# Kernel tuning notes

Hardware: AMD Instinct MI355X
Metric: run time of the kernel (lower is better)

The kernel has to match this reference:

```python
import jax, jax.numpy as jnp
import numpy as np
from jax import lax

C = 256
K = 7
PAD = (K - 1) // 2
EMB = 128
MULT = 4
HID = C * MULT
B = 16
L = 4096
EPS = 1e-6
LAYER_SCALE_INIT = 1e-6


def setup_inputs() -> dict:
    key = jax.random.key(0)
    ks = jax.random.split(key, 10)
    x = jax.random.normal(ks[0], (B, C, L), dtype=jnp.float32)
    t = jax.random.normal(ks[1], (B, EMB), dtype=jnp.float32)
    # depthwise conv: Conv1d(C, C, K, groups=C) -> weight [C, 1, K]
    dw_w = jax.random.normal(ks[2], (C, 1, K), dtype=jnp.float32) * 0.1
    dw_b = jax.random.normal(ks[3], (C,), dtype=jnp.float32) * 0.02
    # FiLM linear: Linear(EMB, 2C)
    film_w = jax.random.normal(ks[4], (2 * C, EMB), dtype=jnp.float32) * 0.05
    film_b = jax.random.normal(ks[5], (2 * C,), dtype=jnp.float32) * 0.02
    # pointwise 1x1 convs
    pw1_w = jax.random.normal(ks[6], (HID, C), dtype=jnp.float32) * 0.05
    pw1_b = jax.random.normal(ks[7], (HID,), dtype=jnp.float32) * 0.02
    pw2_w = jax.random.normal(ks[8], (C, HID), dtype=jnp.float32) * 0.05
    pw2_b = jax.random.normal(ks[9], (C,), dtype=jnp.float32) * 0.02
    gamma = jnp.full((C, 1), LAYER_SCALE_INIT, dtype=jnp.float32)
    return {"x": x, "t": t, "dw_w": dw_w, "dw_b": dw_b,
            "film_w": film_w, "film_b": film_b,
            "pw1_w": pw1_w, "pw1_b": pw1_b,
            "pw2_w": pw2_w, "pw2_b": pw2_b, "gamma": gamma}


def reference(x, t, dw_w, dw_b, film_w, film_b, pw1_w, pw1_b, pw2_w, pw2_b, gamma):
    # circular pad on spatial dim, then valid depthwise conv
    xp = jnp.concatenate([x[..., -PAD:], x, x[..., :PAD]], axis=-1)  # [B, C, L+2*PAD]
    y = lax.conv_general_dilated(
        xp, dw_w, window_strides=(1,), padding='VALID',
        dimension_numbers=('NCH', 'OIH', 'NCH'),
        feature_group_count=C) + dw_b[:, None]                       # [B, C, L]
    # GroupNorm(1, C, affine=False): normalize over (C, L) per sample
    mu = jnp.mean(y, axis=(1, 2), keepdims=True)
    var = jnp.mean(jnp.square(y - mu), axis=(1, 2), keepdims=True)
    yn = (y - mu) * lax.rsqrt(var + EPS)
    # FiLM: scale/shift from embedded time
    ss = t @ film_w.T + film_b                                       # [B, 2C]
    scale, shift = jnp.split(ss, 2, axis=1)                          # [B, C] each
    yn = yn * (scale[:, :, None] + 1.0) + shift[:, :, None]
    # pointwise mixing with ReLU
    h = jax.nn.relu(jnp.einsum('bcl,dc->bdl', yn, pw1_w) + pw1_b[:, None])  # [B, HID, L]
    branch = jnp.einsum('bdl,cd->bcl', h, pw2_w) + pw2_b[:, None]           # [B, C, L]
    # layerscale + residual
    return x + branch * gamma
```

## Files before the change

### kernel.cpp

```cpp
#include <hip/hip_runtime.h>

typedef short s16x8 __attribute__((ext_vector_type(8)));
typedef short s16x4 __attribute__((ext_vector_type(4)));
typedef float f32x4 __attribute__((ext_vector_type(4)));

#define NB 16
#define NC 256
#define NL 4096
#define NH 1024
#define NE 128

#define WS_YNT   0ull
#define WS_PW1   33554432ull
#define WS_PW2   34078720ull
#define WS_AF    34603008ull
#define WS_BF    34619392ull
#define WS_SUMS  34635776ull

#define MFMA16(a, b, c) __builtin_amdgcn_mfma_f32_16x16x32_bf16((a), (b), (c), 0, 0, 0)

static __device__ __forceinline__ short f2bf(float f) {
    unsigned int u = __float_as_uint(f);
    u = (u + 0x7fffu + ((u >> 16) & 1u)) >> 16;
    return (short)u;
}
static __device__ __forceinline__ float bf2f(short s) {
    return __uint_as_float(((unsigned int)(unsigned short)s) << 16);
}

__global__ __launch_bounds__(256) void k0_prep(const float* __restrict__ pw1,
                                               const float* __restrict__ pw2,
                                               short* __restrict__ pw1b,
                                               short* __restrict__ pw2b,
                                               float* __restrict__ sums) {
    int idx = blockIdx.x * 256 + threadIdx.x;
    if (idx < NH * NC) {
        pw1b[idx] = f2bf(pw1[idx]);
        pw2b[idx] = f2bf(pw2[idx]);
    }
    if (blockIdx.x == 0 && threadIdx.x < 32) sums[threadIdx.x] = 0.f;
}

__global__ __launch_bounds__(256) void k1_dwconv(const float* __restrict__ x,
                                                 const float* __restrict__ dw_w,
                                                 const float* __restrict__ dw_b,
                                                 short* __restrict__ ynt,
                                                 float* __restrict__ sums) {
    __shared__ float xt[64][81];
    __shared__ float red1[4], red2[4];
    const int b = blockIdx.x >> 8;
    const int rem = blockIdx.x & 255;
    const int c0 = (rem >> 6) << 6;
    const int l0 = (rem & 63) << 6;
    const int t = threadIdx.x;

    const float* xb = x + ((size_t)(b * NC + c0)) * NL;
    {
#pragma unroll
        for (int j = 0; j < 5; ++j) {
            const int idx = t + 256 * j;
            const int row = idx / 20;
            const int col = idx - row * 20;
            const int lg = (l0 - 4 + col * 4) & (NL - 1);
            const float4 v = *(const float4*)(xb + (size_t)row * NL + lg);
            xt[row][col * 4 + 0] = v.x;
            xt[row][col * 4 + 1] = v.y;
            xt[row][col * 4 + 2] = v.z;
            xt[row][col * 4 + 3] = v.w;
        }
    }

    const int c = t & 63;
    const int w = t >> 6;
    const float w0 = dw_w[(c0 + c) * 7 + 0], w1 = dw_w[(c0 + c) * 7 + 1],
                w2 = dw_w[(c0 + c) * 7 + 2], w3 = dw_w[(c0 + c) * 7 + 3],
                w4 = dw_w[(c0 + c) * 7 + 4], w5 = dw_w[(c0 + c) * 7 + 5],
                w6 = dw_w[(c0 + c) * 7 + 6];
    const float bb = dw_b[c0 + c];
    __syncthreads();

    float win0 = xt[c][w * 16 + 1], win1 = xt[c][w * 16 + 2], win2 = xt[c][w * 16 + 3],
          win3 = xt[c][w * 16 + 4], win4 = xt[c][w * 16 + 5], win5 = xt[c][w * 16 + 6],
          win6 = xt[c][w * 16 + 7];
    float s1 = 0.f, s2 = 0.f;
    short* yo = ynt + ((size_t)(b * NL + l0 + w * 16)) * NC + c0 + c;
#pragma unroll
    for (int i = 0; i < 16; ++i) {
        const float y = bb + w0 * win0 + w1 * win1 + w2 * win2 + w3 * win3 +
                        w4 * win4 + w5 * win5 + w6 * win6;
        s1 += y;
        s2 += y * y;
        yo[(size_t)i * NC] = f2bf(y);
        win0 = win1; win1 = win2; win2 = win3; win3 = win4; win4 = win5; win5 = win6;
        win6 = xt[c][w * 16 + i + 8];
    }
    for (int off = 32; off; off >>= 1) {
        s1 += __shfl_down(s1, off, 64);
        s2 += __shfl_down(s2, off, 64);
    }
    if ((t & 63) == 0) { red1[w] = s1; red2[w] = s2; }
    __syncthreads();
    if (t == 0) {
        atomicAdd(&sums[b * 2 + 0], red1[0] + red1[1] + red1[2] + red1[3]);
        atomicAdd(&sums[b * 2 + 1], red2[0] + red2[1] + red2[2] + red2[3]);
    }
}

__global__ __launch_bounds__(256) void k2_finalize(const float* __restrict__ tin,
                                                   const float* __restrict__ fw,
                                                   const float* __restrict__ fb,
                                                   const float* __restrict__ sums,
                                                   float* __restrict__ afilm,
                                                   float* __restrict__ bfilm) {
    const int b = blockIdx.x;
    const int c = threadIdx.x;
    const float n = (float)(NC * NL);
    const float mu = sums[2 * b] / n;
    const float var = sums[2 * b + 1] / n - mu * mu;
    const float rs = rsqrtf(var + 1e-6f);

    const f32x4* tv = (const f32x4*)(tin + b * NE);
    const f32x4* wA = (const f32x4*)(fw + (size_t)c * NE);
    const f32x4* wB = (const f32x4*)(fw + (size_t)(NC + c) * NE);
    float sc = 0.f, sh = 0.f;
#pragma unroll
    for (int e = 0; e < NE / 4; ++e) {
        f32x4 tq = tv[e], aq = wA[e], bq = wB[e];
        sc += tq[0] * aq[0] + tq[1] * aq[1] + tq[2] * aq[2] + tq[3] * aq[3];
        sh += tq[0] * bq[0] + tq[1] * bq[1] + tq[2] * bq[2] + tq[3] * bq[3];
    }
    sc += fb[c];
    sh += fb[NC + c];
    const float A = rs * (1.f + sc);
    afilm[b * NC + c] = A;
    bfilm[b * NC + c] = sh - mu * A;
}

__global__ __launch_bounds__(256, 2) void k3_gemm(
    const short* __restrict__ ynt, const short* __restrict__ pw1b,
    const short* __restrict__ pw2b, const float* __restrict__ pb1,
    const float* __restrict__ pb2, const float* __restrict__ afilm,
    const float* __restrict__ bfilm, const float* __restrict__ gamma,
    const float* __restrict__ x, float* __restrict__ out) {
    __shared__ short yn[64 * 264];
    __shared__ short hs[2][64 * 136];

    const int b = blockIdx.x >> 6;
    const int l0 = (blockIdx.x & 63) << 6;
    const int t = threadIdx.x;
    const int lane = t & 63, wid = t >> 6;
    const int ln = lane & 15, quad = lane >> 4;

    {
        const int c8 = (t & 31) * 8;
        const int lrow = t >> 5;
        const f32x4 a0 = *(const f32x4*)(afilm + b * NC + c8);
        const f32x4 a1 = *(const f32x4*)(afilm + b * NC + c8 + 4);
        const f32x4 f0 = *(const f32x4*)(bfilm + b * NC + c8);
        const f32x4 f1 = *(const f32x4*)(bfilm + b * NC + c8 + 4);
        const short* ys = ynt + ((size_t)(b * NL + l0)) * NC + c8;
#pragma unroll
        for (int p = 0; p < 8; ++p) {
            const int l = p * 8 + lrow;
            s16x8 v = *(const s16x8*)(ys + (size_t)l * NC);
            s16x8 o;
#pragma unroll
            for (int j = 0; j < 4; ++j) {
                o[j]     = f2bf(a0[j] * bf2f(v[j])     + f0[j]);
                o[4 + j] = f2bf(a1[j] * bf2f(v[4 + j]) + f1[j]);
            }
            *(s16x8*)(yn + l * 264 + c8) = o;
        }
    }

    const short* A1b = pw1b + (size_t)(32 * wid + ln) * NC + quad * 8;
    const short* A2b = pw2b + (size_t)(64 * wid + ln) * NH + quad * 8;

    s16x8 a1p[16];
#pragma unroll
    for (int kk = 0; kk < 4; ++kk) {
        a1p[2 * kk + 0] = *(const s16x8*)(A1b + kk * 32);
        a1p[2 * kk + 1] = *(const s16x8*)(A1b + 16 * NC + kk * 32);
    }
    __syncthreads();
#pragma unroll
    for (int kk = 4; kk < 8; ++kk) {
        a1p[2 * kk + 0] = *(const s16x8*)(A1b + kk * 32);
        a1p[2 * kk + 1] = *(const s16x8*)(A1b + 16 * NC + kk * 32);
    }

    f32x4 acc1[2][4] = {};
#pragma unroll
    for (int kk = 0; kk < 8; ++kk) {
        const int kq = kk * 32 + quad * 8;
        s16x8 b0 = *(const s16x8*)(yn + (0 * 16 + ln) * 264 + kq);
        s16x8 b1 = *(const s16x8*)(yn + (1 * 16 + ln) * 264 + kq);
        s16x8 b2 = *(const s16x8*)(yn + (2 * 16 + ln) * 264 + kq);
        s16x8 b3 = *(const s16x8*)(yn + (3 * 16 + ln) * 264 + kq);
        acc1[0][0] = MFMA16(a1p[2 * kk], b0, acc1[0][0]);
        acc1[0][1] = MFMA16(a1p[2 * kk], b1, acc1[0][1]);
        acc1[0][2] = MFMA16(a1p[2 * kk], b2, acc1[0][2]);
        acc1[0][3] = MFMA16(a1p[2 * kk], b3, acc1[0][3]);
        acc1[1][0] = MFMA16(a1p[2 * kk + 1], b0, acc1[1][0]);
        acc1[1][1] = MFMA16(a1p[2 * kk + 1], b1, acc1[1][1]);
        acc1[1][2] = MFMA16(a1p[2 * kk + 1], b2, acc1[1][2]);
        acc1[1][3] = MFMA16(a1p[2 * kk + 1], b3, acc1[1][3]);
    }

    f32x4 acc2[4][4] = {};

#pragma unroll 1
    for (int ch = 0; ch < 7; ++ch) {
        const int dc0 = ch * 128;
        s16x8 a2p[16];
        const short* A2 = A2b + dc0;
#pragma unroll
        for (int kk = 0; kk < 4; ++kk) {
#pragma unroll
            for (int m = 0; m < 4; ++m) {
                a2p[4 * kk + m] = *(const s16x8*)(A2 + m * 16 * NH + kk * 32);
            }
        }
        short* hw = &hs[ch & 1][0];
#pragma unroll
        for (int mf = 0; mf < 2; ++mf) {
            const int dbase = 32 * wid + mf * 16 + quad * 4;
            const f32x4 b1v = *(const f32x4*)(pb1 + dc0 + dbase);
#pragma unroll
            for (int nf = 0; nf < 4; ++nf) {
                const int l = nf * 16 + ln;
                s16x4 hv;
#pragma unroll
                for (int r = 0; r < 4; ++r) {
                    hv[r] = f2bf(fmaxf(acc1[mf][nf][r] + b1v[r], 0.f));
                }
                *(s16x4*)(hw + l * 136 + dbase) = hv;
            }
        }
        __syncthreads();
        const short* A1n = A1b + (size_t)(dc0 + 128) * NC;
#pragma unroll
        for (int kk = 0; kk < 4; ++kk) {
            a1p[2 * kk + 0] = *(const s16x8*)(A1n + kk * 32);
            a1p[2 * kk + 1] = *(const s16x8*)(A1n + 16 * NC + kk * 32);
        }
        const short* hr = &hs[ch & 1][0];
#pragma unroll
        for (int kk = 0; kk < 4; ++kk) {
            const int kq = kk * 32 + quad * 8;
            s16x8 h0 = *(const s16x8*)(hr + (0 * 16 + ln) * 136 + kq);
            s16x8 h1 = *(const s16x8*)(hr + (1 * 16 + ln) * 136 + kq);
            s16x8 h2 = *(const s16x8*)(hr + (2 * 16 + ln) * 136 + kq);
            s16x8 h3 = *(const s16x8*)(hr + (3 * 16 + ln) * 136 + kq);
            acc2[0][0] = MFMA16(a2p[4 * kk + 0], h0, acc2[0][0]);
            acc2[0][1] = MFMA16(a2p[4 * kk + 0], h1, acc2[0][1]);
            acc2[0][2] = MFMA16(a2p[4 * kk + 0], h2, acc2[0][2]);
            acc2[0][3] = MFMA16(a2p[4 * kk + 0], h3, acc2[0][3]);
            acc2[1][0] = MFMA16(a2p[4 * kk + 1], h0, acc2[1][0]);
            acc2[1][1] = MFMA16(a2p[4 * kk + 1], h1, acc2[1][1]);
            acc2[1][2] = MFMA16(a2p[4 * kk + 1], h2, acc2[1][2]);
            acc2[1][3] = MFMA16(a2p[4 * kk + 1], h3, acc2[1][3]);
            acc2[2][0] = MFMA16(a2p[4 * kk + 2], h0, acc2[2][0]);
            acc2[2][1] = MFMA16(a2p[4 * kk + 2], h1, acc2[2][1]);
            acc2[2][2] = MFMA16(a2p[4 * kk + 2], h2, acc2[2][2]);
            acc2[2][3] = MFMA16(a2p[4 * kk + 2], h3, acc2[2][3]);
            acc2[3][0] = MFMA16(a2p[4 * kk + 3], h0, acc2[3][0]);
            acc2[3][1] = MFMA16(a2p[4 * kk + 3], h1, acc2[3][1]);
            acc2[3][2] = MFMA16(a2p[4 * kk + 3], h2, acc2[3][2]);
            acc2[3][3] = MFMA16(a2p[4 * kk + 3], h3, acc2[3][3]);
        }
#pragma unroll
        for (int kk = 4; kk < 8; ++kk) {
            a1p[2 * kk + 0] = *(const s16x8*)(A1n + kk * 32);
            a1p[2 * kk + 1] = *(const s16x8*)(A1n + 16 * NC + kk * 32);
        }
#pragma unroll
        for (int i = 0; i < 2; ++i)
#pragma unroll
            for (int j = 0; j < 4; ++j) acc1[i][j] = (f32x4){0.f, 0.f, 0.f, 0.f};
#pragma unroll
        for (int kk = 0; kk < 8; ++kk) {
            const int kq = kk * 32 + quad * 8;
            s16x8 b0 = *(const s16x8*)(yn + (0 * 16 + ln) * 264 + kq);
            s16x8 b1 = *(const s16x8*)(yn + (1 * 16 + ln) * 264 + kq);
            s16x8 b2 = *(const s16x8*)(yn + (2 * 16 + ln) * 264 + kq);
            s16x8 b3 = *(const s16x8*)(yn + (3 * 16 + ln) * 264 + kq);
            acc1[0][0] = MFMA16(a1p[2 * kk], b0, acc1[0][0]);
            acc1[0][1] = MFMA16(a1p[2 * kk], b1, acc1[0][1]);
            acc1[0][2] = MFMA16(a1p[2 * kk], b2, acc1[0][2]);
            acc1[0][3] = MFMA16(a1p[2 * kk], b3, acc1[0][3]);
            acc1[1][0] = MFMA16(a1p[2 * kk + 1], b0, acc1[1][0]);
            acc1[1][1] = MFMA16(a1p[2 * kk + 1], b1, acc1[1][1]);
            acc1[1][2] = MFMA16(a1p[2 * kk + 1], b2, acc1[1][2]);
            acc1[1][3] = MFMA16(a1p[2 * kk + 1], b3, acc1[1][3]);
        }
    }

    {
        const int dc0 = 7 * 128;
        s16x8 a2p[16];
        const short* A2 = A2b + dc0;
#pragma unroll
        for (int kk = 0; kk < 4; ++kk) {
#pragma unroll
            for (int m = 0; m < 4; ++m) {
                a2p[4 * kk + m] = *(const s16x8*)(A2 + m * 16 * NH + kk * 32);
            }
        }
        short* hw = &hs[1][0];
#pragma unroll
        for (int mf = 0; mf < 2; ++mf) {
            const int dbase = 32 * wid + mf * 16 + quad * 4;
            const f32x4 b1v = *(const f32x4*)(pb1 + dc0 + dbase);
#pragma unroll
            for (int nf = 0; nf < 4; ++nf) {
                const int l = nf * 16 + ln;
                s16x4 hv;
#pragma unroll
                for (int r = 0; r < 4; ++r) {
                    hv[r] = f2bf(fmaxf(acc1[mf][nf][r] + b1v[r], 0.f));
                }
                *(s16x4*)(hw + l * 136 + dbase) = hv;
            }
        }
        __syncthreads();
        const short* hr = &hs[1][0];
#pragma unroll
        for (int kk = 0; kk < 4; ++kk) {
            const int kq = kk * 32 + quad * 8;
            s16x8 h0 = *(const s16x8*)(hr + (0 * 16 + ln) * 136 + kq);
            s16x8 h1 = *(const s16x8*)(hr + (1 * 16 + ln) * 136 + kq);
            s16x8 h2 = *(const s16x8*)(hr + (2 * 16 + ln) * 136 + kq);
            s16x8 h3 = *(const s16x8*)(hr + (3 * 16 + ln) * 136 + kq);
            acc2[0][0] = MFMA16(a2p[4 * kk + 0], h0, acc2[0][0]);
            acc2[0][1] = MFMA16(a2p[4 * kk + 0], h1, acc2[0][1]);
            acc2[0][2] = MFMA16(a2p[4 * kk + 0], h2, acc2[0][2]);
            acc2[0][3] = MFMA16(a2p[4 * kk + 0], h3, acc2[0][3]);
            acc2[1][0] = MFMA16(a2p[4 * kk + 1], h0, acc2[1][0]);
            acc2[1][1] = MFMA16(a2p[4 * kk + 1], h1, acc2[1][1]);
            acc2[1][2] = MFMA16(a2p[4 * kk + 1], h2, acc2[1][2]);
            acc2[1][3] = MFMA16(a2p[4 * kk + 1], h3, acc2[1][3]);
            acc2[2][0] = MFMA16(a2p[4 * kk + 2], h0, acc2[2][0]);
            acc2[2][1] = MFMA16(a2p[4 * kk + 2], h1, acc2[2][1]);
            acc2[2][2] = MFMA16(a2p[4 * kk + 2], h2, acc2[2][2]);
            acc2[2][3] = MFMA16(a2p[4 * kk + 2], h3, acc2[2][3]);
            acc2[3][0] = MFMA16(a2p[4 * kk + 3], h0, acc2[3][0]);
            acc2[3][1] = MFMA16(a2p[4 * kk + 3], h1, acc2[3][1]);
            acc2[3][2] = MFMA16(a2p[4 * kk + 3], h2, acc2[3][2]);
            acc2[3][3] = MFMA16(a2p[4 * kk + 3], h3, acc2[3][3]);
        }
    }

#pragma unroll
    for (int mf2 = 0; mf2 < 4; ++mf2) {
        const int cbase = 64 * wid + mf2 * 16 + quad * 4;
        const f32x4 g4 = *(const f32x4*)(gamma + cbase);
        const f32x4 b4 = *(const f32x4*)(pb2 + cbase);
#pragma unroll
        for (int r = 0; r < 4; ++r) {
            const int c = cbase + r;
            const size_t base = ((size_t)(b * NC + c)) * NL + l0 + ln;
            const float* xr = x + base;
            float* orow = out + base;
#pragma unroll
            for (int nf2 = 0; nf2 < 4; ++nf2) {
                orow[nf2 * 16] = xr[nf2 * 16] + g4[r] * (acc2[mf2][nf2][r] + b4[r]);
            }
        }
    }
}

extern "C" void kernel_launch(void* const* d_in, const int* in_sizes, int n_in,
                              void* d_out, int out_size, void* d_ws, size_t ws_size,
                              hipStream_t stream) {
    (void)in_sizes; (void)n_in; (void)out_size; (void)ws_size;
    const float* x      = (const float*)d_in[0];
    const float* tin    = (const float*)d_in[1];
    const float* dw_w   = (const float*)d_in[2];
    const float* dw_b   = (const float*)d_in[3];
    const float* film_w = (const float*)d_in[4];
    const float* film_b = (const float*)d_in[5];
    const float* pw1_w  = (const float*)d_in[6];
    const float* pw1_b  = (const float*)d_in[7];
    const float* pw2_w  = (const float*)d_in[8];
    const float* pw2_b  = (const float*)d_in[9];
    const float* gamma  = (const float*)d_in[10];
    float* out = (float*)d_out;

    char* ws = (char*)d_ws;
    short* ynt  = (short*)(ws + WS_YNT);
    short* pw1b = (short*)(ws + WS_PW1);
    short* pw2b = (short*)(ws + WS_PW2);
    float* afilm = (float*)(ws + WS_AF);
    float* bfilm = (float*)(ws + WS_BF);
    float* sums  = (float*)(ws + WS_SUMS);

    hipLaunchKernelGGL(k0_prep, dim3(1024), dim3(256), 0, stream,
                       pw1_w, pw2_w, pw1b, pw2b, sums);
    hipLaunchKernelGGL(k1_dwconv, dim3(NB * 256), dim3(256), 0, stream,
                       x, dw_w, dw_b, ynt, sums);
    hipLaunchKernelGGL(k2_finalize, dim3(NB), dim3(256), 0, stream,
                       tin, film_w, film_b, sums, afilm, bfilm);
    hipLaunchKernelGGL(k3_gemm, dim3(NB * (NL / 64)), dim3(256), 0, stream,
                       ynt, pw1b, pw2b, pw1_b, pw2_b, afilm, bfilm, gamma, x, out);
}
```

Baseline: 336.9 us.

## Single-buffer hidden tile, raise occupancy to 3 blocks, add MFMA priority hints

Replaces the double-buffered hidden-activation LDS tile with a single buffer and adds a second barrier per chunk so the buffer can be reused. This cuts LDS per block so that launch bounds can request 3 blocks per CU instead of 2. The peeled final chunk is folded into the loop behind ch<7 guards, and s_setprio is raised around the MFMA sections. Risks are the extra barrier per chunk and register spills under the tighter per-thread register budget.

```diff
diff --git a/kernel.cpp b/kernel.cpp
--- a/kernel.cpp
+++ b/kernel.cpp
@@ -136,14 +136,14 @@
     bfilm[b * NC + c] = sh - mu * A;
 }
 
-__global__ __launch_bounds__(256, 2) void k3_gemm(
+__global__ __launch_bounds__(256, 3) void k3_gemm(
     const short* __restrict__ ynt, const short* __restrict__ pw1b,
     const short* __restrict__ pw2b, const float* __restrict__ pb1,
     const float* __restrict__ pb2, const float* __restrict__ afilm,
     const float* __restrict__ bfilm, const float* __restrict__ gamma,
     const float* __restrict__ x, float* __restrict__ out) {
     __shared__ short yn[64 * 264];
-    __shared__ short hs[2][64 * 136];
+    __shared__ short hs[64 * 136];
 
     const int b = blockIdx.x >> 6;
     const int l0 = (blockIdx.x & 63) << 6;
@@ -190,6 +190,7 @@
     }
 
     f32x4 acc1[2][4] = {};
+    __builtin_amdgcn_s_setprio(1);
 #pragma unroll
     for (int kk = 0; kk < 8; ++kk) {
         const int kq = kk * 32 + quad * 8;
@@ -206,11 +207,12 @@
         acc1[1][2] = MFMA16(a1p[2 * kk + 1], b2, acc1[1][2]);
         acc1[1][3] = MFMA16(a1p[2 * kk + 1], b3, acc1[1][3]);
     }
+    __builtin_amdgcn_s_setprio(0);
 
     f32x4 acc2[4][4] = {};
 
 #pragma unroll 1
-    for (int ch = 0; ch < 7; ++ch) {
+    for (int ch = 0; ch < 8; ++ch) {
         const int dc0 = ch * 128;
         s16x8 a2p[16];
         const short* A2 = A2b + dc0;
@@ -221,7 +223,6 @@
                 a2p[4 * kk + m] = *(const s16x8*)(A2 + m * 16 * NH + kk * 32);
             }
         }
-        short* hw = &hs[ch & 1][0];
 #pragma unroll
         for (int mf = 0; mf < 2; ++mf) {
             const int dbase = 32 * wid + mf * 16 + quad * 4;
@@ -234,24 +235,27 @@
                 for (int r = 0; r < 4; ++r) {
                     hv[r] = f2bf(fmaxf(acc1[mf][nf][r] + b1v[r], 0.f));
                 }
-                *(s16x4*)(hw + l * 136 + dbase) = hv;
+                *(s16x4*)(hs + l * 136 + dbase) = hv;
             }
         }
         __syncthreads();
+
         const short* A1n = A1b + (size_t)(dc0 + 128) * NC;
-#pragma unroll
-        for (int kk = 0; kk < 4; ++kk) {
-            a1p[2 * kk + 0] = *(const s16x8*)(A1n + kk * 32);
-            a1p[2 * kk + 1] = *(const s16x8*)(A1n + 16 * NC + kk * 32);
-        }
-        const short* hr = &hs[ch & 1][0];
+        if (ch < 7) {
+#pragma unroll
+            for (int kk = 0; kk < 4; ++kk) {
+                a1p[2 * kk + 0] = *(const s16x8*)(A1n + kk * 32);
+                a1p[2 * kk + 1] = *(const s16x8*)(A1n + 16 * NC + kk * 32);
+            }
+        }
+        __builtin_amdgcn_s_setprio(1);
 #pragma unroll
         for (int kk = 0; kk < 4; ++kk) {
             const int kq = kk * 32 + quad * 8;
-            s16x8 h0 = *(const s16x8*)(hr + (0 * 16 + ln) * 136 + kq);
-            s16x8 h1 = *(const s16x8*)(hr + (1 * 16 + ln) * 136 + kq);
-            s16x8 h2 = *(const s16x8*)(hr + (2 * 16 + ln) * 136 + kq);
-            s16x8 h3 = *(const s16x8*)(hr + (3 * 16 + ln) * 136 + kq);
+            s16x8 h0 = *(const s16x8*)(hs + (0 * 16 + ln) * 136 + kq);
+            s16x8 h1 = *(const s16x8*)(hs + (1 * 16 + ln) * 136 + kq);
+            s16x8 h2 = *(const s16x8*)(hs + (2 * 16 + ln) * 136 + kq);
+            s16x8 h3 = *(const s16x8*)(hs + (3 * 16 + ln) * 136 + kq);
             acc2[0][0] = MFMA16(a2p[4 * kk + 0], h0, acc2[0][0]);
             acc2[0][1] = MFMA16(a2p[4 * kk + 0], h1, acc2[0][1]);
             acc2[0][2] = MFMA16(a2p[4 * kk + 0], h2, acc2[0][2]);
@@ -269,85 +273,39 @@
             acc2[3][2] = MFMA16(a2p[4 * kk + 3], h2, acc2[3][2]);
             acc2[3][3] = MFMA16(a2p[4 * kk + 3], h3, acc2[3][3]);
         }
-#pragma unroll
-        for (int kk = 4; kk < 8; ++kk) {
-            a1p[2 * kk + 0] = *(const s16x8*)(A1n + kk * 32);
-            a1p[2 * kk + 1] = *(const s16x8*)(A1n + 16 * NC + kk * 32);
-        }
-#pragma unroll
-        for (int i = 0; i < 2; ++i)
-#pragma unroll
-            for (int j = 0; j < 4; ++j) acc1[i][j] = (f32x4){0.f, 0.f, 0.f, 0.f};
-#pragma unroll
-        for (int kk = 0; kk < 8; ++kk) {
-            const int kq = kk * 32 + quad * 8;
-            s16x8 b0 = *(const s16x8*)(yn + (0 * 16 + ln) * 264 + kq);
-            s16x8 b1 = *(const s16x8*)(yn + (1 * 16 + ln) * 264 + kq);
-            s16x8 b2 = *(const s16x8*)(yn + (2 * 16 + ln) * 264 + kq);
-            s16x8 b3 = *(const s16x8*)(yn + (3 * 16 + ln) * 264 + kq);
-            acc1[0][0] = MFMA16(a1p[2 * kk], b0, acc1[0][0]);
-            acc1[0][1] = MFMA16(a1p[2 * kk], b1, acc1[0][1]);
-            acc1[0][2] = MFMA16(a1p[2 * kk], b2, acc1[0][2]);
-            acc1[0][3] = MFMA16(a1p[2 * kk], b3, acc1[0][3]);
-            acc1[1][0] = MFMA16(a1p[2 * kk + 1], b0, acc1[1][0]);
-            acc1[1][1] = MFMA16(a1p[2 * kk + 1], b1, acc1[1][1]);
-            acc1[1][2] = MFMA16(a1p[2 * kk + 1], b2, acc1[1][2]);
-            acc1[1][3] = MFMA16(a1p[2 * kk + 1], b3, acc1[1][3]);
-        }
-    }
-
-    {
-        const int dc0 = 7 * 128;
-        s16x8 a2p[16];
-        const short* A2 = A2b + dc0;
-#pragma unroll
-        for (int kk = 0; kk < 4; ++kk) {
-#pragma unroll
-            for (int m = 0; m < 4; ++m) {
-                a2p[4 * kk + m] = *(const s16x8*)(A2 + m * 16 * NH + kk * 32);
-            }
-        }
-        short* hw = &hs[1][0];
-#pragma unroll
-        for (int mf = 0; mf < 2; ++mf) {
-            const int dbase = 32 * wid + mf * 16 + quad * 4;
-            const f32x4 b1v = *(const f32x4*)(pb1 + dc0 + dbase);
-#pragma unroll
-            for (int nf = 0; nf < 4; ++nf) {
-                const int l = nf * 16 + ln;
-                s16x4 hv;
-#pragma unroll
-                for (int r = 0; r < 4; ++r) {
-                    hv[r] = f2bf(fmaxf(acc1[mf][nf][r] + b1v[r], 0.f));
-                }
-                *(s16x4*)(hw + l * 136 + dbase) = hv;
+        __builtin_amdgcn_s_setprio(0);
+        if (ch < 7) {
+#pragma unroll
+            for (int kk = 4; kk < 8; ++kk) {
+                a1p[2 * kk + 0] = *(const s16x8*)(A1n + kk * 32);
+                a1p[2 * kk + 1] = *(const s16x8*)(A1n + 16 * NC + kk * 32);
             }
         }
         __syncthreads();
-        const short* hr = &hs[1][0];
-#pragma unroll
-        for (int kk = 0; kk < 4; ++kk) {
-            const int kq = kk * 32 + quad * 8;
-            s16x8 h0 = *(const s16x8*)(hr + (0 * 16 + ln) * 136 + kq);
-            s16x8 h1 = *(const s16x8*)(hr + (1 * 16 + ln) * 136 + kq);
-            s16x8 h2 = *(const s16x8*)(hr + (2 * 16 + ln) * 136 + kq);
-            s16x8 h3 = *(const s16x8*)(hr + (3 * 16 + ln) * 136 + kq);
-            acc2[0][0] = MFMA16(a2p[4 * kk + 0], h0, acc2[0][0]);
-            acc2[0][1] = MFMA16(a2p[4 * kk + 0], h1, acc2[0][1]);
-            acc2[0][2] = MFMA16(a2p[4 * kk + 0], h2, acc2[0][2]);
-            acc2[0][3] = MFMA16(a2p[4 * kk + 0], h3, acc2[0][3]);
-            acc2[1][0] = MFMA16(a2p[4 * kk + 1], h0, acc2[1][0]);
-            acc2[1][1] = MFMA16(a2p[4 * kk + 1], h1, acc2[1][1]);
-            acc2[1][2] = MFMA16(a2p[4 * kk + 1], h2, acc2[1][2]);
-            acc2[1][3] = MFMA16(a2p[4 * kk + 1], h3, acc2[1][3]);
-            acc2[2][0] = MFMA16(a2p[4 * kk + 2], h0, acc2[2][0]);
-            acc2[2][1] = MFMA16(a2p[4 * kk + 2], h1, acc2[2][1]);
-            acc2[2][2] = MFMA16(a2p[4 * kk + 2], h2, acc2[2][2]);
-            acc2[2][3] = MFMA16(a2p[4 * kk + 2], h3, acc2[2][3]);
-            acc2[3][0] = MFMA16(a2p[4 * kk + 3], h0, acc2[3][0]);
-            acc2[3][1] = MFMA16(a2p[4 * kk + 3], h1, acc2[3][1]);
-            acc2[3][2] = MFMA16(a2p[4 * kk + 3], h2, acc2[3][2]);
-            acc2[3][3] = MFMA16(a2p[4 * kk + 3], h3, acc2[3][3]);
+
+        if (ch < 7) {
+#pragma unroll
+            for (int i = 0; i < 2; ++i)
+#pragma unroll
+                for (int j = 0; j < 4; ++j) acc1[i][j] = (f32x4){0.f, 0.f, 0.f, 0.f};
+            __builtin_amdgcn_s_setprio(1);
+#pragma unroll
+            for (int kk = 0; kk < 8; ++kk) {
+                const int kq = kk * 32 + quad * 8;
+                s16x8 b0 = *(const s16x8*)(yn + (0 * 16 + ln) * 264 + kq);
+                s16x8 b1 = *(const s16x8*)(yn + (1 * 16 + ln) * 264 + kq);
+                s16x8 b2 = *(const s16x8*)(yn + (2 * 16 + ln) * 264 + kq);
+                s16x8 b3 = *(const s16x8*)(yn + (3 * 16 + ln) * 264 + kq);
+                acc1[0][0] = MFMA16(a1p[2 * kk], b0, acc1[0][0]);
+                acc1[0][1] = MFMA16(a1p[2 * kk], b1, acc1[0][1]);
+                acc1[0][2] = MFMA16(a1p[2 * kk], b2, acc1[0][2]);
+                acc1[0][3] = MFMA16(a1p[2 * kk], b3, acc1[0][3]);
+                acc1[1][0] = MFMA16(a1p[2 * kk + 1], b0, acc1[1][0]);
+                acc1[1][1] = MFMA16(a1p[2 * kk + 1], b1, acc1[1][1]);
+                acc1[1][2] = MFMA16(a1p[2 * kk + 1], b2, acc1[1][2]);
+                acc1[1][3] = MFMA16(a1p[2 * kk + 1], b3, acc1[1][3]);
+            }
+            __builtin_amdgcn_s_setprio(0);
         }
     }
 
```

Result: slower. 548.7 us (+62.9%).
